# Performance work log

Measured on AMD Instinct MI355X. Metric: run time of the kernel, lower is better.

Reference implementation:

```python
import jax, jax.numpy as jnp
import numpy as np

B, D, Q = 64, 1024, 128
V, E, H = 50000, 300, 256   # vocab, embed_dim, prealign hidden
POS_V, POS_D = 56, 12
NER_V, NER_D = 19, 8


def setup_inputs() -> dict:
    key = jax.random.key(0)
    ks = jax.random.split(key, 10)
    word_emb = (jax.random.normal(ks[0], (V, E), jnp.float32) * 0.1).at[0].set(0.0)
    pos_emb = (jax.random.normal(ks[1], (POS_V, POS_D), jnp.float32) * 0.1).at[0].set(0.0)
    ner_emb = (jax.random.normal(ks[2], (NER_V, NER_D), jnp.float32) * 0.1).at[0].set(0.0)
    proj_w = jax.random.normal(ks[3], (E, H), jnp.float32) / np.sqrt(E)
    proj_b = jnp.zeros((H,), jnp.float32)
    return {
        "query_tok": jax.random.randint(ks[4], (B, Q), 0, V),
        "doc_tok": jax.random.randint(ks[5], (B, D), 0, V),
        "doc_pos": jax.random.randint(ks[6], (B, D), 0, POS_V),
        "doc_ner": jax.random.randint(ks[7], (B, D), 0, NER_V),
        "doc_fea": jax.random.normal(ks[8], (B, D, 4), jnp.float32),
        "word_emb": word_emb,
        "proj_w": proj_w,
        "proj_b": proj_b,
        "pos_emb": pos_emb,
        "ner_emb": ner_emb,
    }


def _embed(table, idx):
    # padding_idx=0 semantics: row 0 contributes zeros
    return table[idx] * (idx != 0)[..., None].astype(table.dtype)


def reference(query_tok, doc_tok, doc_pos, doc_ner, doc_fea,
              word_emb, proj_w, proj_b, pos_emb, ner_emb):
    doc_e = _embed(word_emb, doc_tok)      # [B,D,E]
    query_e = _embed(word_emb, query_tok)  # [B,Q,E]

    # Prealign: shared Linear+ReLU proj, then bmm -> softmax -> bmm
    d_proj = jax.nn.relu(doc_e @ proj_w + proj_b)    # [B,D,H]
    q_proj = jax.nn.relu(query_e @ proj_w + proj_b)  # [B,Q,H]
    scores = jnp.einsum('bdh,bqh->bdq', d_proj, q_proj)
    attn = jax.nn.softmax(scores, axis=-1)           # softmax over query dim
    prealign = jnp.einsum('bdq,bqe->bde', attn, query_e)  # [B,D,E]

    doc_out = jnp.concatenate(
        [doc_e, prealign, _embed(ner_emb, doc_ner), _embed(pos_emb, doc_pos), doc_fea],
        axis=-1)  # [B,D,E+E+8+12+4]
    return query_e, doc_out
```

## Files before the change

kernel.cpp:

```cpp
#include <hip/hip_runtime.h>
#include <hip/hip_bf16.h>

typedef unsigned short u16;
typedef __attribute__((ext_vector_type(8))) short bf16x8;
typedef __attribute__((ext_vector_type(4))) float f32x4;

#define MFMA16(a, b, c) __builtin_amdgcn_mfma_f32_16x16x32_bf16((a), (b), (c), 0, 0, 0)

#define NB 64
#define ND 1024
#define NQ 128
#define NE 300
#define NH 256
#define KP 320
#define QETN 304
#define DOC_W 624

static __device__ __forceinline__ u16 f2bf(float f) {
  union { __bf16 h; u16 u; } c; c.h = (__bf16)f; return c.u;
}

static __device__ __forceinline__ bf16x8 pack8(float4 f0, float4 f1) {
  union { bf16x8 v; u16 u[8]; } r;
  r.u[0] = f2bf(f0.x); r.u[1] = f2bf(f0.y); r.u[2] = f2bf(f0.z); r.u[3] = f2bf(f0.w);
  r.u[4] = f2bf(f1.x); r.u[5] = f2bf(f1.y); r.u[6] = f2bf(f1.z); r.u[7] = f2bf(f1.w);
  return r.v;
}

static __device__ __forceinline__ bf16x8 cvt8(const float* p) {
  return pack8(*(const float4*)p, *(const float4*)(p + 4));
}

__global__ void k_aux(const float* __restrict__ w, u16* __restrict__ wt,
                      const int* __restrict__ qtok, const float* __restrict__ table,
                      float* __restrict__ q_out,
                      const int* __restrict__ ner, const int* __restrict__ pos,
                      const float* __restrict__ fea,
                      const float* __restrict__ ner_emb, const float* __restrict__ pos_emb,
                      float* __restrict__ doc_out) {
  int bx = blockIdx.x;
  if (bx < 320) {
    int idx = bx * 256 + threadIdx.x;
    int n = idx / KP, k = idx % KP;
    wt[idx] = (k < NE) ? f2bf(w[k * NH + n]) : (u16)0;
  } else if (bx < 2720) {
    int idx = (bx - 320) * 256 + threadIdx.x;
    int row = idx / 75, j = idx % 75;
    int k = j * 4;
    float4 v = {0.f, 0.f, 0.f, 0.f};
    int t = qtok[row];
    if (t != 0) v = *(const float4*)(table + (long)t * NE + k);
    *(float4*)(q_out + (long)row * NE + k) = v;
  } else {
    int idx = (bx - 2720) * 256 + threadIdx.x;
    int row = idx / 6, c0 = (idx % 6) * 4;
    float4 v;
    float* vp = (float*)&v;
#pragma unroll
    for (int u = 0; u < 4; ++u) {
      int c = c0 + u;
      float x;
      if (c < 8)       { int t = ner[row]; x = t ? ner_emb[t * 8 + c] : 0.f; }
      else if (c < 20) { int t = pos[row]; x = t ? pos_emb[t * 12 + (c - 8)] : 0.f; }
      else             { x = fea[(long)row * 4 + (c - 20)]; }
      vp[u] = x;
    }
    *(float4*)(doc_out + (long)row * DOC_W + 600 + c0) = v;
  }
}

__launch_bounds__(256)
__global__ void k_qside(const float* __restrict__ qo, const u16* __restrict__ Wt,
                        const float* __restrict__ bias,
                        u16* __restrict__ qP, u16* __restrict__ qet) {
  __shared__ u16 T[64][314];
  int tid = threadIdx.x;
  if (blockIdx.x < 128) {
    int l = tid & 63, w = tid >> 6;
    int lr = l & 15, lg = l >> 4;
    int bm = blockIdx.x * 64 + (w & 1) * 32;
    int bn = (w >> 1) * 128;
    f32x4 acc[2][8] = {};
    const float* xp0 = qo + (long)(bm + lr) * NE + 8 * lg;
    const float* xp1 = xp0 + 16 * NE;
    const u16* wp = Wt + (long)(bn + lr) * KP + 8 * lg;
#pragma unroll 2
    for (int ks = 0; ks < KP; ks += 32) {
      bf16x8 a0 = cvt8(xp0 + ks);
      bf16x8 a1 = cvt8(xp1 + ks);
#pragma unroll
      for (int nt = 0; nt < 8; ++nt) {
        bf16x8 b0 = *(const bf16x8*)(wp + (long)nt * 16 * KP + ks);
        acc[0][nt] = MFMA16(a0, b0, acc[0][nt]);
        acc[1][nt] = MFMA16(a1, b0, acc[1][nt]);
      }
    }
#pragma unroll
    for (int nt = 0; nt < 8; ++nt) {
      int col = bn + nt * 16 + lr;
      float bv = bias[col];
#pragma unroll
      for (int mt = 0; mt < 2; ++mt)
#pragma unroll
        for (int r = 0; r < 4; ++r) {
          int row = bm + mt * 16 + 4 * lg + r;
          float v = acc[mt][nt][r] + bv;
          v = v > 0.f ? v : 0.f;
          qP[(long)row * NH + col] = f2bf(v);
        }
    }
  } else {
    int bx = blockIdx.x - 128;
    int b = bx >> 1, k0 = (bx & 1) * 64;
    const float* src = qo + ((long)b * NQ + k0) * NE;
    for (int i = tid; i < 64 * 75; i += 256) {
      int row = i / 75, j = (i % 75) * 4;
      float4 f = *(const float4*)(src + (long)row * NE + j);
      T[row][j]     = f2bf(f.x); T[row][j + 1] = f2bf(f.y);
      T[row][j + 2] = f2bf(f.z); T[row][j + 3] = f2bf(f.w);
    }
    __syncthreads();
    u16* dst = qet + (long)b * QETN * NQ + k0;
    for (int i = tid; i < QETN * 16; i += 256) {
      int n = i / 16, kq = (i % 16) * 4;
      u16 v[4] = {0, 0, 0, 0};
      if (n < NE) {
        v[0] = T[kq][n]; v[1] = T[kq + 1][n]; v[2] = T[kq + 2][n]; v[3] = T[kq + 3][n];
      }
      *(uint2*)(dst + (long)n * NQ + kq) = *(const uint2*)v;
    }
  }
}

__launch_bounds__(256, 2)
__global__ void k_fused(const int* __restrict__ dtok, const float* __restrict__ emb,
                        float* doc_out, const u16* __restrict__ Wt,
                        const float* __restrict__ bias,
                        const u16* __restrict__ qP, const u16* __restrict__ qeT) {
  __shared__ __align__(16) u16 dp[128][264];
  u16 (*p_lds)[136] = (u16 (*)[136]) & dp[0][0];
  int bid = blockIdx.x;
  int xcd = bid & 7, j = bid >> 3;
  int b = xcd * 8 + (j >> 3);
  int chunk = j & 7;
  int l = threadIdx.x & 63, w = threadIdx.x >> 6;
  int lr = l & 15, lg = l >> 4;
  long blkrow = (long)b * ND + chunk * 128;

  {
    int mrow0 = (w & 1) * 64;
    int ncol0 = (w >> 1) * 128;
    bool wr = (w >> 1) == 0;
    const float* arow[4];
    float* drow[4];
#pragma unroll
    for (int mt = 0; mt < 4; ++mt) {
      long r = blkrow + mrow0 + mt * 16 + lr;
      arow[mt] = emb + (long)dtok[r] * NE;
      drow[mt] = doc_out + r * DOC_W;
    }
    const u16* wp = Wt + (long)(ncol0 + lr) * KP + 8 * lg;
    f32x4 acc[4][8] = {};
    int c0 = 8 * lg;
#pragma unroll 3
    for (int ks = 0; ks < 288; ks += 32) {
      bf16x8 a[4];
#pragma unroll
      for (int mt = 0; mt < 4; ++mt) {
        int col = ks + c0;
        float4 f0 = *(const float4*)(arow[mt] + col);
        float4 f1 = *(const float4*)(arow[mt] + col + 4);
        if (wr) {
          *(float4*)(drow[mt] + col) = f0;
          *(float4*)(drow[mt] + col + 4) = f1;
        }
        a[mt] = pack8(f0, f1);
      }
#pragma unroll
      for (int nt = 0; nt < 8; ++nt) {
        bf16x8 bb = *(const bf16x8*)(wp + nt * 16 * KP + ks);
#pragma unroll
        for (int mt = 0; mt < 4; ++mt) acc[mt][nt] = MFMA16(a[mt], bb, acc[mt][nt]);
      }
    }
    {
      const int ks = 288;
      int col = ks + c0;
      float4 z = {0.f, 0.f, 0.f, 0.f};
      bf16x8 a[4];
#pragma unroll
      for (int mt = 0; mt < 4; ++mt) {
        float4 f0 = (col + 4 <= NE) ? *(const float4*)(arow[mt] + col) : z;
        float4 f1 = (col + 8 <= NE) ? *(const float4*)(arow[mt] + col + 4) : z;
        if (wr) {
          if (col + 4 <= NE) *(float4*)(drow[mt] + col) = f0;
          if (col + 8 <= NE) *(float4*)(drow[mt] + col + 4) = f1;
        }
        a[mt] = pack8(f0, f1);
      }
#pragma unroll
      for (int nt = 0; nt < 8; ++nt) {
        bf16x8 bb = *(const bf16x8*)(wp + nt * 16 * KP + ks);
#pragma unroll
        for (int mt = 0; mt < 4; ++mt) acc[mt][nt] = MFMA16(a[mt], bb, acc[mt][nt]);
      }
    }
#pragma unroll
    for (int nt = 0; nt < 8; ++nt) {
      int col = ncol0 + nt * 16 + lr;
      float bv = bias[col];
#pragma unroll
      for (int mt = 0; mt < 4; ++mt)
#pragma unroll
        for (int r = 0; r < 4; ++r) {
          float v = acc[mt][nt][r] + bv;
          dp[mrow0 + mt * 16 + 4 * lg + r][col] = f2bf(v > 0.f ? v : 0.f);
        }
    }
  }
  __syncthreads();

  f32x4 s[2][8] = {};
  {
    const u16* qpp = qP + ((long)b * NQ + lr) * NH + 8 * lg;
#pragma unroll
    for (int ks = 0; ks < NH; ks += 32) {
      bf16x8 a0 = *(const bf16x8*)&dp[w * 32 + lr][ks + 8 * lg];
      bf16x8 a1 = *(const bf16x8*)&dp[w * 32 + 16 + lr][ks + 8 * lg];
#pragma unroll
      for (int nt = 0; nt < 8; ++nt) {
        bf16x8 bb = *(const bf16x8*)(qpp + (long)nt * 16 * NH + ks);
        s[0][nt] = MFMA16(a0, bb, s[0][nt]);
        s[1][nt] = MFMA16(a1, bb, s[1][nt]);
      }
    }
  }
  __syncthreads();

#pragma unroll
  for (int mt = 0; mt < 2; ++mt) {
    f32x4 mx;
#pragma unroll
    for (int r = 0; r < 4; ++r) {
      float m = s[mt][0][r];
#pragma unroll
      for (int nt = 1; nt < 8; ++nt) m = fmaxf(m, s[mt][nt][r]);
      mx[r] = m;
    }
#pragma unroll
    for (int d = 1; d < 16; d <<= 1)
#pragma unroll
      for (int r = 0; r < 4; ++r) mx[r] = fmaxf(mx[r], __shfl_xor(mx[r], d));
    f32x4 sum = {};
#pragma unroll
    for (int nt = 0; nt < 8; ++nt)
#pragma unroll
      for (int r = 0; r < 4; ++r) {
        float p = __expf(s[mt][nt][r] - mx[r]);
        s[mt][nt][r] = p;
        sum[r] += p;
      }
#pragma unroll
    for (int d = 1; d < 16; d <<= 1)
#pragma unroll
      for (int r = 0; r < 4; ++r) sum[r] += __shfl_xor(sum[r], d);
    f32x4 inv;
#pragma unroll
    for (int r = 0; r < 4; ++r) inv[r] = 1.0f / sum[r];
#pragma unroll
    for (int nt = 0; nt < 8; ++nt)
#pragma unroll
      for (int r = 0; r < 4; ++r)
        p_lds[w * 32 + mt * 16 + 4 * lg + r][nt * 16 + lr] = f2bf(s[mt][nt][r] * inv[r]);
  }

  const u16* qtp = qeT + (long)b * QETN * NQ;
  bf16x8 pa[2][4];
#pragma unroll
  for (int mt = 0; mt < 2; ++mt)
#pragma unroll
    for (int ksi = 0; ksi < 4; ++ksi)
      pa[mt][ksi] = *(const bf16x8*)&p_lds[w * 32 + mt * 16 + lr][ksi * 32 + 8 * lg];
#pragma unroll 2
  for (int nt = 0; nt < 19; ++nt) {
    f32x4 acc0 = {}, acc1 = {};
#pragma unroll
    for (int ksi = 0; ksi < 4; ++ksi) {
      bf16x8 bb = *(const bf16x8*)(qtp + (long)(nt * 16 + lr) * NQ + ksi * 32 + 8 * lg);
      acc0 = MFMA16(pa[0][ksi], bb, acc0);
      acc1 = MFMA16(pa[1][ksi], bb, acc1);
    }
    int col = nt * 16 + lr;
    if (col < NE) {
#pragma unroll
      for (int r = 0; r < 4; ++r) {
        long rl0 = blkrow + w * 32 + 4 * lg + r;
        doc_out[rl0 * DOC_W + 300 + col] = acc0[r];
        doc_out[(rl0 + 16) * DOC_W + 300 + col] = acc1[r];
      }
    }
  }
}

extern "C" void kernel_launch(void* const* d_in, const int* in_sizes, int n_in,
                              void* d_out, int out_size, void* d_ws, size_t ws_size,
                              hipStream_t stream) {
  const int *query_tok = nullptr, *doc_tok = nullptr, *doc_pos = nullptr, *doc_ner = nullptr;
  const float *doc_fea = nullptr, *word_emb = nullptr, *proj_w = nullptr,
              *proj_b = nullptr, *pos_emb = nullptr, *ner_emb = nullptr;
  int n65536 = 0;
  for (int i = 0; i < n_in; ++i) {
    switch (in_sizes[i]) {
      case 15000000: word_emb  = (const float*)d_in[i]; break;
      case 262144:   doc_fea   = (const float*)d_in[i]; break;
      case 76800:    proj_w    = (const float*)d_in[i]; break;
      case 8192:     query_tok = (const int*)d_in[i];   break;
      case 256:      proj_b    = (const float*)d_in[i]; break;
      case 672:      pos_emb   = (const float*)d_in[i]; break;
      case 152:      ner_emb   = (const float*)d_in[i]; break;
      case 65536:
        if (n65536 == 0)      doc_tok = (const int*)d_in[i];
        else if (n65536 == 1) doc_pos = (const int*)d_in[i];
        else                  doc_ner = (const int*)d_in[i];
        ++n65536; break;
      default: break;
    }
  }

  float* out = (float*)d_out;
  float* q_out   = out;
  float* doc_out = out + (size_t)NB * NQ * NE;

  char* ws = (char*)d_ws;
  u16* Wt  = (u16*)ws; ws += (size_t)NH * KP * 2;
  u16* qP  = (u16*)ws; ws += (size_t)NB * NQ * NH * 2;
  u16* qeT = (u16*)ws; ws += (size_t)NB * QETN * NQ * 2;

  k_aux<<<dim3(4256), dim3(256), 0, stream>>>(
      proj_w, Wt, query_tok, word_emb, q_out,
      doc_ner, doc_pos, doc_fea, ner_emb, pos_emb, doc_out);
  k_qside<<<dim3(256), dim3(256), 0, stream>>>(q_out, Wt, proj_b, qP, qeT);
  k_fused<<<dim3(512), dim3(256), 0, stream>>>(
      doc_tok, word_emb, doc_out, Wt, proj_b, qP, qeT);
}
```

Baseline: 128.1 us.

## Halve fused doc tile to 64 rows and double grid for occupancy

The fused doc kernel now processes 64 document rows per block instead of 128. That halves the LDS tile and the per-wave accumulator arrays, and launch bounds rise to 4 blocks per SM. The grid doubles to 1024 blocks to give more parallelism and better latency hiding on the gathered embedding loads. In exchange, each Wt column tile and the qP/qeT operands are re-read by twice as many blocks, and each embedding row now feeds only 64 output columns per wave, which lowers reuse.

```diff
diff --git a/kernel.cpp b/kernel.cpp
--- a/kernel.cpp
+++ b/kernel.cpp
@@ -132,36 +132,35 @@
   }
 }
 
-__launch_bounds__(256, 2)
+__launch_bounds__(256, 4)
 __global__ void k_fused(const int* __restrict__ dtok, const float* __restrict__ emb,
                         float* doc_out, const u16* __restrict__ Wt,
                         const float* __restrict__ bias,
                         const u16* __restrict__ qP, const u16* __restrict__ qeT) {
-  __shared__ __align__(16) u16 dp[128][264];
+  __shared__ __align__(16) u16 dp[64][264];
   u16 (*p_lds)[136] = (u16 (*)[136]) & dp[0][0];
   int bid = blockIdx.x;
   int xcd = bid & 7, j = bid >> 3;
-  int b = xcd * 8 + (j >> 3);
-  int chunk = j & 7;
+  int b = xcd * 8 + (j >> 4);
+  int chunk = j & 15;
   int l = threadIdx.x & 63, w = threadIdx.x >> 6;
   int lr = l & 15, lg = l >> 4;
-  long blkrow = (long)b * ND + chunk * 128;
+  long blkrow = (long)b * ND + chunk * 64;
+  int c0 = 8 * lg;
 
   {
-    int mrow0 = (w & 1) * 64;
-    int ncol0 = (w >> 1) * 128;
-    bool wr = (w >> 1) == 0;
+    int ncol0 = w * 64;
+    bool wr = (w == 0);
     const float* arow[4];
     float* drow[4];
 #pragma unroll
     for (int mt = 0; mt < 4; ++mt) {
-      long r = blkrow + mrow0 + mt * 16 + lr;
+      long r = blkrow + mt * 16 + lr;
       arow[mt] = emb + (long)dtok[r] * NE;
       drow[mt] = doc_out + r * DOC_W;
     }
-    const u16* wp = Wt + (long)(ncol0 + lr) * KP + 8 * lg;
-    f32x4 acc[4][8] = {};
-    int c0 = 8 * lg;
+    const u16* wp = Wt + (long)(ncol0 + lr) * KP + c0;
+    f32x4 acc[4][4] = {};
 #pragma unroll 3
     for (int ks = 0; ks < 288; ks += 32) {
       bf16x8 a[4];
@@ -177,7 +176,7 @@
         a[mt] = pack8(f0, f1);
       }
 #pragma unroll
-      for (int nt = 0; nt < 8; ++nt) {
+      for (int nt = 0; nt < 4; ++nt) {
         bf16x8 bb = *(const bf16x8*)(wp + nt * 16 * KP + ks);
 #pragma unroll
         for (int mt = 0; mt < 4; ++mt) acc[mt][nt] = MFMA16(a[mt], bb, acc[mt][nt]);
@@ -199,14 +198,14 @@
         a[mt] = pack8(f0, f1);
       }
 #pragma unroll
-      for (int nt = 0; nt < 8; ++nt) {
+      for (int nt = 0; nt < 4; ++nt) {
         bf16x8 bb = *(const bf16x8*)(wp + nt * 16 * KP + ks);
 #pragma unroll
         for (int mt = 0; mt < 4; ++mt) acc[mt][nt] = MFMA16(a[mt], bb, acc[mt][nt]);
       }
     }
 #pragma unroll
-    for (int nt = 0; nt < 8; ++nt) {
+    for (int nt = 0; nt < 4; ++nt) {
       int col = ncol0 + nt * 16 + lr;
       float bv = bias[col];
 #pragma unroll
@@ -214,37 +213,34 @@
 #pragma unroll
         for (int r = 0; r < 4; ++r) {
           float v = acc[mt][nt][r] + bv;
-          dp[mrow0 + mt * 16 + 4 * lg + r][col] = f2bf(v > 0.f ? v : 0.f);
+          dp[mt * 16 + 4 * lg + r][col] = f2bf(v > 0.f ? v : 0.f);
         }
     }
   }
   __syncthreads();
 
-  f32x4 s[2][8] = {};
+  f32x4 s[8] = {};
   {
     const u16* qpp = qP + ((long)b * NQ + lr) * NH + 8 * lg;
 #pragma unroll
     for (int ks = 0; ks < NH; ks += 32) {
-      bf16x8 a0 = *(const bf16x8*)&dp[w * 32 + lr][ks + 8 * lg];
-      bf16x8 a1 = *(const bf16x8*)&dp[w * 32 + 16 + lr][ks + 8 * lg];
+      bf16x8 a0 = *(const bf16x8*)&dp[w * 16 + lr][ks + 8 * lg];
 #pragma unroll
       for (int nt = 0; nt < 8; ++nt) {
         bf16x8 bb = *(const bf16x8*)(qpp + (long)nt * 16 * NH + ks);
-        s[0][nt] = MFMA16(a0, bb, s[0][nt]);
-        s[1][nt] = MFMA16(a1, bb, s[1][nt]);
+        s[nt] = MFMA16(a0, bb, s[nt]);
       }
     }
   }
   __syncthreads();
 
-#pragma unroll
-  for (int mt = 0; mt < 2; ++mt) {
+  {
     f32x4 mx;
 #pragma unroll
     for (int r = 0; r < 4; ++r) {
-      float m = s[mt][0][r];
-#pragma unroll
-      for (int nt = 1; nt < 8; ++nt) m = fmaxf(m, s[mt][nt][r]);
+      float m = s[0][r];
+#pragma unroll
+      for (int nt = 1; nt < 8; ++nt) m = fmaxf(m, s[nt][r]);
       mx[r] = m;
     }
 #pragma unroll
@@ -256,8 +252,8 @@
     for (int nt = 0; nt < 8; ++nt)
 #pragma unroll
       for (int r = 0; r < 4; ++r) {
-        float p = __expf(s[mt][nt][r] - mx[r]);
-        s[mt][nt][r] = p;
+        float p = __expf(s[nt][r] - mx[r]);
+        s[nt][r] = p;
         sum[r] += p;
       }
 #pragma unroll
@@ -271,33 +267,27 @@
     for (int nt = 0; nt < 8; ++nt)
 #pragma unroll
       for (int r = 0; r < 4; ++r)
-        p_lds[w * 32 + mt * 16 + 4 * lg + r][nt * 16 + lr] = f2bf(s[mt][nt][r] * inv[r]);
+        p_lds[w * 16 + 4 * lg + r][nt * 16 + lr] = f2bf(s[nt][r] * inv[r]);
   }
 
   const u16* qtp = qeT + (long)b * QETN * NQ;
-  bf16x8 pa[2][4];
-#pragma unroll
-  for (int mt = 0; mt < 2; ++mt)
-#pragma unroll
-    for (int ksi = 0; ksi < 4; ++ksi)
-      pa[mt][ksi] = *(const bf16x8*)&p_lds[w * 32 + mt * 16 + lr][ksi * 32 + 8 * lg];
+  bf16x8 pa[4];
+#pragma unroll
+  for (int ksi = 0; ksi < 4; ++ksi)
+    pa[ksi] = *(const bf16x8*)&p_lds[w * 16 + lr][ksi * 32 + c0];
 #pragma unroll 2
   for (int nt = 0; nt < 19; ++nt) {
-    f32x4 acc0 = {}, acc1 = {};
+    f32x4 acc0 = {};
 #pragma unroll
     for (int ksi = 0; ksi < 4; ++ksi) {
-      bf16x8 bb = *(const bf16x8*)(qtp + (long)(nt * 16 + lr) * NQ + ksi * 32 + 8 * lg);
-      acc0 = MFMA16(pa[0][ksi], bb, acc0);
-      acc1 = MFMA16(pa[1][ksi], bb, acc1);
+      bf16x8 bb = *(const bf16x8*)(qtp + (long)(nt * 16 + lr) * NQ + ksi * 32 + c0);
+      acc0 = MFMA16(pa[ksi], bb, acc0);
     }
     int col = nt * 16 + lr;
     if (col < NE) {
 #pragma unroll
-      for (int r = 0; r < 4; ++r) {
-        long rl0 = blkrow + w * 32 + 4 * lg + r;
-        doc_out[rl0 * DOC_W + 300 + col] = acc0[r];
-        doc_out[(rl0 + 16) * DOC_W + 300 + col] = acc1[r];
-      }
+      for (int r = 0; r < 4; ++r)
+        doc_out[(blkrow + w * 16 + 4 * lg + r) * DOC_W + 300 + col] = acc0[r];
     }
   }
 }
@@ -340,6 +330,6 @@
       proj_w, Wt, query_tok, word_emb, q_out,
       doc_ner, doc_pos, doc_fea, ner_emb, pos_emb, doc_out);
   k_qside<<<dim3(256), dim3(256), 0, stream>>>(q_out, Wt, proj_b, qP, qeT);
-  k_fused<<<dim3(512), dim3(256), 0, stream>>>(
+  k_fused<<<dim3(1024), dim3(256), 0, stream>>>(
       doc_tok, word_emb, doc_out, Wt, proj_b, qP, qeT);
 }
```

Result: slower. 198.5 us (+54.9%).

## Merge aux and query-side kernels into one launch that gathers embeddings directly

Applied to the files above, without the earlier changes.

Folds the weight transpose, query gather, aux features, query-embedding transpose and query projection into a single 1024-thread kernel. The query-side blocks gather straight from the embedding table instead of waiting on q_out. Each projection block transposes its own 64-column slice of proj_w into shared memory, which drops the dependency between kernels. This removes one launch and a serialization point. The cost is redundant weight conversion in every projection block, a larger block size, and a smaller MFMA tile per wave.

```diff
diff --git a/kernel.cpp b/kernel.cpp
--- a/kernel.cpp
+++ b/kernel.cpp
@@ -27,32 +27,29 @@
   return r.v;
 }
 
-static __device__ __forceinline__ bf16x8 cvt8(const float* p) {
-  return pack8(*(const float4*)p, *(const float4*)(p + 4));
-}
-
-__global__ void k_aux(const float* __restrict__ w, u16* __restrict__ wt,
-                      const int* __restrict__ qtok, const float* __restrict__ table,
-                      float* __restrict__ q_out,
+__global__ void k_pre(const float* __restrict__ w, u16* __restrict__ wt,
+                      const int* __restrict__ qtok, const float* __restrict__ emb,
+                      float* __restrict__ q_out, u16* __restrict__ qet,
                       const int* __restrict__ ner, const int* __restrict__ pos,
                       const float* __restrict__ fea,
                       const float* __restrict__ ner_emb, const float* __restrict__ pos_emb,
-                      float* __restrict__ doc_out) {
-  int bx = blockIdx.x;
-  if (bx < 320) {
-    int idx = bx * 256 + threadIdx.x;
+                      float* __restrict__ doc_out,
+                      const float* __restrict__ bias, u16* __restrict__ qP) {
+  __shared__ u16 T[64][322];
+  int bx = blockIdx.x, tid = threadIdx.x;
+  if (bx < 80) {
+    int idx = bx * 1024 + tid;
     int n = idx / KP, k = idx % KP;
     wt[idx] = (k < NE) ? f2bf(w[k * NH + n]) : (u16)0;
-  } else if (bx < 2720) {
-    int idx = (bx - 320) * 256 + threadIdx.x;
-    int row = idx / 75, j = idx % 75;
-    int k = j * 4;
+  } else if (bx < 680) {
+    int idx = (bx - 80) * 1024 + tid;
+    int row = idx / 75, j = (idx % 75) * 4;
     float4 v = {0.f, 0.f, 0.f, 0.f};
     int t = qtok[row];
-    if (t != 0) v = *(const float4*)(table + (long)t * NE + k);
-    *(float4*)(q_out + (long)row * NE + k) = v;
-  } else {
-    int idx = (bx - 2720) * 256 + threadIdx.x;
+    if (t != 0) v = *(const float4*)(emb + (long)t * NE + j);
+    *(float4*)(q_out + (long)row * NE + j) = v;
+  } else if (bx < 1064) {
+    int idx = (bx - 680) * 1024 + tid;
     int row = idx / 6, c0 = (idx % 6) * 4;
     float4 v;
     float* vp = (float*)&v;
@@ -66,68 +63,76 @@
       vp[u] = x;
     }
     *(float4*)(doc_out + (long)row * DOC_W + 600 + c0) = v;
-  }
-}
-
-__launch_bounds__(256)
-__global__ void k_qside(const float* __restrict__ qo, const u16* __restrict__ Wt,
-                        const float* __restrict__ bias,
-                        u16* __restrict__ qP, u16* __restrict__ qet) {
-  __shared__ u16 T[64][314];
-  int tid = threadIdx.x;
-  if (blockIdx.x < 128) {
-    int l = tid & 63, w = tid >> 6;
-    int lr = l & 15, lg = l >> 4;
-    int bm = blockIdx.x * 64 + (w & 1) * 32;
-    int bn = (w >> 1) * 128;
-    f32x4 acc[2][8] = {};
-    const float* xp0 = qo + (long)(bm + lr) * NE + 8 * lg;
-    const float* xp1 = xp0 + 16 * NE;
-    const u16* wp = Wt + (long)(bn + lr) * KP + 8 * lg;
-#pragma unroll 2
-    for (int ks = 0; ks < KP; ks += 32) {
-      bf16x8 a0 = cvt8(xp0 + ks);
-      bf16x8 a1 = cvt8(xp1 + ks);
-#pragma unroll
-      for (int nt = 0; nt < 8; ++nt) {
-        bf16x8 b0 = *(const bf16x8*)(wp + (long)nt * 16 * KP + ks);
-        acc[0][nt] = MFMA16(a0, b0, acc[0][nt]);
-        acc[1][nt] = MFMA16(a1, b0, acc[1][nt]);
-      }
-    }
-#pragma unroll
-    for (int nt = 0; nt < 8; ++nt) {
-      int col = bn + nt * 16 + lr;
-      float bv = bias[col];
-#pragma unroll
-      for (int mt = 0; mt < 2; ++mt)
-#pragma unroll
-        for (int r = 0; r < 4; ++r) {
-          int row = bm + mt * 16 + 4 * lg + r;
-          float v = acc[mt][nt][r] + bv;
-          v = v > 0.f ? v : 0.f;
-          qP[(long)row * NH + col] = f2bf(v);
-        }
-    }
-  } else {
-    int bx = blockIdx.x - 128;
-    int b = bx >> 1, k0 = (bx & 1) * 64;
-    const float* src = qo + ((long)b * NQ + k0) * NE;
-    for (int i = tid; i < 64 * 75; i += 256) {
+  } else if (bx < 1192) {
+    int bxx = bx - 1064;
+    int b = bxx >> 1, k0 = (bxx & 1) * 64;
+    for (int i = tid; i < 64 * 75; i += 1024) {
       int row = i / 75, j = (i % 75) * 4;
-      float4 f = *(const float4*)(src + (long)row * NE + j);
+      int t = qtok[b * NQ + k0 + row];
+      float4 f = {0.f, 0.f, 0.f, 0.f};
+      if (t != 0) f = *(const float4*)(emb + (long)t * NE + j);
       T[row][j]     = f2bf(f.x); T[row][j + 1] = f2bf(f.y);
       T[row][j + 2] = f2bf(f.z); T[row][j + 3] = f2bf(f.w);
     }
     __syncthreads();
     u16* dst = qet + (long)b * QETN * NQ + k0;
-    for (int i = tid; i < QETN * 16; i += 256) {
+    for (int i = tid; i < QETN * 16; i += 1024) {
       int n = i / 16, kq = (i % 16) * 4;
       u16 v[4] = {0, 0, 0, 0};
       if (n < NE) {
         v[0] = T[kq][n]; v[1] = T[kq + 1][n]; v[2] = T[kq + 2][n]; v[3] = T[kq + 3][n];
       }
       *(uint2*)(dst + (long)n * NQ + kq) = *(const uint2*)v;
+    }
+  } else {
+    int bx2 = bx - 1192;
+    int rowg = bx2 >> 2, colg = bx2 & 3;
+    int ncol0 = colg * 64;
+    for (int i = tid; i < 300 * 64; i += 1024) {
+      int n = i & 63, k = i >> 6;
+      T[n][k] = f2bf(w[k * NH + ncol0 + n]);
+    }
+    for (int i = tid; i < 64 * 22; i += 1024)
+      T[i / 22][300 + (i % 22)] = 0;
+    __syncthreads();
+    int l = tid & 63, wv = tid >> 6;
+    int lr = l & 15, lg = l >> 4, c0 = 8 * lg;
+    int bm0 = rowg * 256 + wv * 16;
+    const float* ar = emb + (long)qtok[bm0 + lr] * NE;
+    f32x4 acc[4] = {};
+#pragma unroll 3
+    for (int ks = 0; ks < 288; ks += 32) {
+      bf16x8 a0 = pack8(*(const float4*)(ar + ks + c0), *(const float4*)(ar + ks + c0 + 4));
+#pragma unroll
+      for (int nt = 0; nt < 4; ++nt) {
+        bf16x8 bb = *(const bf16x8*)&T[nt * 16 + lr][ks + c0];
+        acc[nt] = MFMA16(a0, bb, acc[nt]);
+      }
+    }
+    {
+      const int ks = 288;
+      int col = ks + c0;
+      float4 z = {0.f, 0.f, 0.f, 0.f};
+      float4 f0 = (col + 4 <= NE) ? *(const float4*)(ar + col) : z;
+      float4 f1 = (col + 8 <= NE) ? *(const float4*)(ar + col + 4) : z;
+      bf16x8 a0 = pack8(f0, f1);
+#pragma unroll
+      for (int nt = 0; nt < 4; ++nt) {
+        bf16x8 bb = *(const bf16x8*)&T[nt * 16 + lr][ks + c0];
+        acc[nt] = MFMA16(a0, bb, acc[nt]);
+      }
+    }
+#pragma unroll
+    for (int nt = 0; nt < 4; ++nt) {
+      int col = ncol0 + nt * 16 + lr;
+      float bv = bias[col];
+#pragma unroll
+      for (int r = 0; r < 4; ++r) {
+        int row = bm0 + 4 * lg + r;
+        float v = acc[nt][r] + bv;
+        v = v > 0.f ? v : 0.f;
+        qP[(long)row * NH + col] = f2bf(v);
+      }
     }
   }
 }
@@ -336,10 +341,9 @@
   u16* qP  = (u16*)ws; ws += (size_t)NB * NQ * NH * 2;
   u16* qeT = (u16*)ws; ws += (size_t)NB * QETN * NQ * 2;
 
-  k_aux<<<dim3(4256), dim3(256), 0, stream>>>(
-      proj_w, Wt, query_tok, word_emb, q_out,
-      doc_ner, doc_pos, doc_fea, ner_emb, pos_emb, doc_out);
-  k_qside<<<dim3(256), dim3(256), 0, stream>>>(q_out, Wt, proj_b, qP, qeT);
+  k_pre<<<dim3(1320), dim3(1024), 0, stream>>>(
+      proj_w, Wt, query_tok, word_emb, q_out, qeT,
+      doc_ner, doc_pos, doc_fea, ner_emb, pos_emb, doc_out, proj_b, qP);
   k_fused<<<dim3(512), dim3(256), 0, stream>>>(
       doc_tok, word_emb, doc_out, Wt, proj_b, qP, qeT);
 }
```

Result: faster. 120.6 us (-5.9%).
